# Kernel optimization log

Hardware: AMD Instinct MI355X
Metric: run time of the kernel (lower is better)

Reference implementation:

```python
import jax, jax.numpy as jnp
import numpy as np

D = 1024      # n_embd
NH = 16       # attention heads
E = 8         # n_experts
K = 2         # k_best
FF = 4 * D    # expert MLP hidden
EPS = 1e-6    # rms_norm_epsilon
TEMP = 1.0    # target_temperature


def setup_inputs() -> dict:
    key = jax.random.key(0)
    ks = jax.random.split(key, 12)
    B, S = 2, 1024
    s = 0.02
    return {
        "x": jax.random.normal(ks[0], (B, S, D), jnp.float32),
        "attn_norm_w": jnp.ones((D,), jnp.float32),
        "wq": jax.random.normal(ks[1], (D, D), jnp.float32) * s,
        "wk": jax.random.normal(ks[2], (D, D), jnp.float32) * s,
        "wv": jax.random.normal(ks[3], (D, D), jnp.float32) * s,
        "wo": jax.random.normal(ks[4], (D, D), jnp.float32) * s,
        "mlp_norm_w": jnp.ones((D,), jnp.float32),
        "router_w": jax.random.normal(ks[5], (D, E), jnp.float32) * s,
        "w1": jax.random.normal(ks[6], (E, D, FF), jnp.float32) * s,
        "b1": jnp.zeros((E, FF), jnp.float32),
        "w2": jax.random.normal(ks[7], (E, FF, D), jnp.float32) * s,
        "b2": jnp.zeros((E, D), jnp.float32),
    }


def _rmsnorm(x, w):
    var = jnp.mean(jnp.square(x), axis=-1, keepdims=True)
    return x * jax.lax.rsqrt(var + EPS) * w


def _attention(x, wq, wk, wv, wo):
    B, S, _ = x.shape
    dh = D // NH
    q = (x @ wq).reshape(B, S, NH, dh)
    k = (x @ wk).reshape(B, S, NH, dh)
    v = (x @ wv).reshape(B, S, NH, dh)
    scores = jnp.einsum("bqhd,bkhd->bhqk", q, k) / jnp.sqrt(jnp.float32(dh))
    causal = jnp.tril(jnp.ones((S, S), bool))  # [S,S]
    scores = jnp.where(causal[None, None], scores, jnp.finfo(scores.dtype).min)
    attn = jax.nn.softmax(scores, axis=-1)
    out = jnp.einsum("bhqk,bkhd->bqhd", attn, v).reshape(B, S, D)
    return out @ wo


def reference(x, attn_norm_w, wq, wk, wv, wo, mlp_norm_w, router_w, w1, b1, w2, b2):
    B, S, _ = x.shape
    # attention sub-block
    x = x + _attention(_rmsnorm(x, attn_norm_w), wq, wk, wv, wo)
    residual = x
    h = _rmsnorm(x, mlp_norm_w)  # [B,S,D]

    # router: temperature softmax + top-k
    logits = h @ router_w / TEMP                      # [B,S,E]
    probs = jax.nn.softmax(logits, axis=-1)
    top_k_scores, top_k_indices = jax.lax.top_k(probs, K)  # [B,S,K]
    onehot = jax.nn.one_hot(top_k_indices, E, dtype=h.dtype)  # [B,S,K,E]
    gates = jnp.einsum("bsk,bske->bse", top_k_scores, onehot)  # [B,S,E]

    # load-balancing loss (Switch-style) + expert counts
    counts = jnp.sum(onehot, axis=(0, 1, 2))          # [E]
    frac = counts / (B * S * K)
    mean_prob = jnp.mean(probs, axis=(0, 1))          # [E]
    balancing_loss = E * jnp.sum(frac * mean_prob)

    # experts: dense dispatch; tokens with zero gate contribute nothing,
    # so this matches the sort/gather/scatter top-k combine exactly.
    pre = jnp.einsum("bsd,edf->ebsf", h, w1) + b1[:, None, None]  # [E,B,S,FF]
    act = jax.nn.gelu(pre)
    y = jnp.einsum("ebsf,efd->ebsd", act, w2) + b2[:, None, None]  # [E,B,S,D]
    moe = jnp.einsum("ebsd,bse->bsd", y, gates)

    out = residual + moe
    return out, balancing_loss, counts
```

## Files before the change

kernel.cpp:

```cpp
#include <hip/hip_runtime.h>

typedef __bf16 bf16;
typedef __bf16 bf16x8 __attribute__((ext_vector_type(8)));
typedef float f32x4 __attribute__((ext_vector_type(4)));

#define D_   1024
#define S_   1024
#define B_   2
#define NTOK 2048
#define FF_  4096
#define NE   8
#define CAP  5120
#define OUTN 2097152

__device__ __forceinline__ float gelu_f(float x) {
    float u = 0.7978845608028654f * (x + 0.044715f * x * x * x);
    float a = fabsf(u);
    float e = __expf(-2.0f * a);
    float t = (1.0f - e) / (1.0f + e);
    t = copysignf(t, u);
    return 0.5f * x * (1.0f + t);
}

__device__ __forceinline__ void gload16(const void* g, void* l) {
    __builtin_amdgcn_global_load_lds((const __attribute__((address_space(1))) unsigned int*)g,
                                     (__attribute__((address_space(3))) unsigned int*)l,
                                     16, 0, 0);
}

__global__ __launch_bounds__(256) void rmsnorm_k(const float* __restrict__ x,
                                                 const float* __restrict__ w,
                                                 float* __restrict__ yf,
                                                 bf16* __restrict__ yhi,
                                                 bf16* __restrict__ ylo) {
    int row = blockIdx.x;
    int t = threadIdx.x;
    const float* xr = x + (size_t)row * D_;
    float4 v = *(const float4*)(xr + t * 4);
    float ss = v.x * v.x + v.y * v.y + v.z * v.z + v.w * v.w;
    for (int off = 32; off; off >>= 1) ss += __shfl_down(ss, off);
    __shared__ float wsum[4];
    if ((t & 63) == 0) wsum[t >> 6] = ss;
    __syncthreads();
    float tot = wsum[0] + wsum[1] + wsum[2] + wsum[3];
    float rr = rsqrtf(tot * (1.0f / D_) + 1e-6f);
    float4 wv = *(const float4*)(w + t * 4);
    float y[4];
    y[0] = v.x * rr * wv.x; y[1] = v.y * rr * wv.y;
    y[2] = v.z * rr * wv.z; y[3] = v.w * rr * wv.w;
    if (yf) *(float4*)(yf + (size_t)row * D_ + t * 4) = *(float4*)y;
    if (yhi) {
#pragma unroll
        for (int i = 0; i < 4; i++) {
            bf16 hi = (bf16)y[i];
            yhi[(size_t)row * D_ + t * 4 + i] = hi;
            if (ylo) ylo[(size_t)row * D_ + t * 4 + i] = (bf16)(y[i] - (float)hi);
        }
    }
}

__global__ __launch_bounds__(256) void trans_split_k(
    const float* __restrict__ w0, const float* __restrict__ w1p,
    const float* __restrict__ w2p, const float* __restrict__ w3,
    bf16* o0h, bf16* o0l, bf16* o1h, bf16* o1l,
    bf16* o2h, bf16* o2l, bf16* o3h, bf16* o3l) {
    int z = blockIdx.z;
    const float* src = (z == 0) ? w0 : (z == 1) ? w1p : (z == 2) ? w2p : w3;
    bf16* dh = (z == 0) ? o0h : (z == 1) ? o1h : (z == 2) ? o2h : o3h;
    bf16* dl = (z == 0) ? o0l : (z == 1) ? o1l : (z == 2) ? o2l : o3l;
    __shared__ float tl[32][33];
    int c0 = blockIdx.x * 32, r0 = blockIdx.y * 32;
    int tx = threadIdx.x & 31, ty = threadIdx.x >> 5;
#pragma unroll
    for (int i = 0; i < 4; i++) {
        int r = ty + i * 8;
        tl[r][tx] = src[(size_t)(r0 + r) * 1024 + c0 + tx];
    }
    __syncthreads();
#pragma unroll
    for (int i = 0; i < 4; i++) {
        int c = ty + i * 8;
        float v = tl[tx][c];
        bf16 hi = (bf16)v;
        dh[(size_t)(c0 + c) * 1024 + r0 + tx] = hi;
        dl[(size_t)(c0 + c) * 1024 + r0 + tx] = (bf16)(v - (float)hi);
    }
}

__global__ __launch_bounds__(256) void transpose_cast_k(const float* __restrict__ in,
                                                        bf16* __restrict__ out,
                                                        int R, int C) {
    __shared__ float tl[32][33];
    size_t base = (size_t)blockIdx.z * R * C;
    const float* src = in + base;
    bf16* dst = out + base;
    int c0 = blockIdx.x * 32, r0 = blockIdx.y * 32;
    int tx = threadIdx.x & 31, tyy = threadIdx.x >> 5;
#pragma unroll
    for (int i = 0; i < 4; i++) {
        int r = tyy + i * 8;
        tl[r][tx] = src[(size_t)(r0 + r) * C + c0 + tx];
    }
    __syncthreads();
#pragma unroll
    for (int i = 0; i < 4; i++) {
        int c = tyy + i * 8;
        dst[(size_t)(c0 + c) * R + r0 + tx] = (bf16)tl[tx][c];
    }
}

#define SPLIT_STAGE(bi, k0)                             \
    gload16(gah0 + (k0), Lah[bi] + wv * 512);           \
    gload16(gah1 + (k0), Lah[bi] + 2048 + wv * 512);    \
    gload16(gal0 + (k0), Lal[bi] + wv * 512);           \
    gload16(gal1 + (k0), Lal[bi] + 2048 + wv * 512);    \
    gload16(gbh0 + (k0), Lbh[bi] + wv * 512);           \
    gload16(gbh1 + (k0), Lbh[bi] + 2048 + wv * 512);    \
    gload16(gbl0 + (k0), Lbl[bi] + wv * 512);           \
    gload16(gbl1 + (k0), Lbl[bi] + 2048 + wv * 512);

#define SPLIT_COMPUTE(bi) {                                                            \
    bf16x8 fah[4], fal[4], fbh[4], fbl[4];                                             \
    _Pragma("unroll") for (int i = 0; i < 4; i++) {                                    \
        fah[i] = *(const bf16x8*)(Lah[bi] + ra_off[i]);                                \
        fal[i] = *(const bf16x8*)(Lal[bi] + ra_off[i]);                                \
        fbh[i] = *(const bf16x8*)(Lbh[bi] + rb_off[i]);                                \
        fbl[i] = *(const bf16x8*)(Lbl[bi] + rb_off[i]);                                \
    }                                                                                  \
    _Pragma("unroll") for (int mt = 0; mt < 4; mt++)                                   \
    _Pragma("unroll") for (int nt = 0; nt < 4; nt++) {                                 \
        acc[mt][nt] = __builtin_amdgcn_mfma_f32_16x16x32_bf16(fah[mt], fbh[nt], acc[mt][nt], 0, 0, 0); \
        acc[mt][nt] = __builtin_amdgcn_mfma_f32_16x16x32_bf16(fah[mt], fbl[nt], acc[mt][nt], 0, 0, 0); \
        acc[mt][nt] = __builtin_amdgcn_mfma_f32_16x16x32_bf16(fal[mt], fbh[nt], acc[mt][nt], 0, 0, 0); \
    } }

#define GEMM128_SPLIT_BODY(EPILOGUE)                                                   \
    __shared__ __align__(16) bf16 Lah[2][4096];                                        \
    __shared__ __align__(16) bf16 Lal[2][4096];                                        \
    __shared__ __align__(16) bf16 Lbh[2][4096];                                        \
    __shared__ __align__(16) bf16 Lbl[2][4096];                                        \
    int t = threadIdx.x;                                                               \
    int wv = t >> 6, ln = t & 63;                                                      \
    int wm = wv >> 1, wn = wv & 1, l15 = ln & 15, qd = ln >> 4;                        \
    int sr0 = t >> 2, sr1 = 64 + sr0, cl = t & 3;                                      \
    int cs0 = (cl ^ ((sr0 >> 1) & 3)) * 8;                                             \
    int cs1 = (cl ^ ((sr1 >> 1) & 3)) * 8;                                             \
    const bf16* gah0 = Ah + (size_t)(m0 + sr0) * 1024 + cs0;                           \
    const bf16* gah1 = Ah + (size_t)(m0 + sr1) * 1024 + cs1;                           \
    const bf16* gal0 = Al + (size_t)(m0 + sr0) * 1024 + cs0;                           \
    const bf16* gal1 = Al + (size_t)(m0 + sr1) * 1024 + cs1;                           \
    const bf16* gbh0 = Bh + (size_t)(n0 + sr0) * 1024 + cs0;                           \
    const bf16* gbh1 = Bh + (size_t)(n0 + sr1) * 1024 + cs1;                           \
    const bf16* gbl0 = Bl + (size_t)(n0 + sr0) * 1024 + cs0;                           \
    const bf16* gbl1 = Bl + (size_t)(n0 + sr1) * 1024 + cs1;                           \
    int ra_off[4], rb_off[4];                                                          \
    _Pragma("unroll") for (int i = 0; i < 4; i++) {                                    \
        int r1 = wm * 64 + i * 16 + l15;                                               \
        ra_off[i] = r1 * 32 + (qd ^ ((r1 >> 1) & 3)) * 8;                              \
        int r2 = wn * 64 + i * 16 + l15;                                               \
        rb_off[i] = r2 * 32 + (qd ^ ((r2 >> 1) & 3)) * 8;                              \
    }                                                                                  \
    f32x4 acc[4][4];                                                                   \
    _Pragma("unroll") for (int mt = 0; mt < 4; mt++)                                   \
    _Pragma("unroll") for (int nt = 0; nt < 4; nt++) acc[mt][nt] = (f32x4){0.f,0.f,0.f,0.f}; \
    SPLIT_STAGE(0, 0);                                                                 \
    __syncthreads();                                                                   \
    for (int k0 = 0; k0 < 1024; k0 += 64) {                                            \
        SPLIT_STAGE(1, k0 + 32);                                                       \
        SPLIT_COMPUTE(0);                                                              \
        __syncthreads();                                                               \
        if (k0 + 64 < 1024) { SPLIT_STAGE(0, k0 + 64); }                               \
        SPLIT_COMPUTE(1);                                                              \
        __syncthreads();                                                               \
    }                                                                                  \
    _Pragma("unroll") for (int mt = 0; mt < 4; mt++)                                   \
    _Pragma("unroll") for (int nt = 0; nt < 4; nt++)                                   \
        _Pragma("unroll") for (int r = 0; r < 4; r++) {                                \
            int gm = m0 + wm * 64 + mt * 16 + qd * 4 + r;                              \
            int gn = n0 + wn * 64 + nt * 16 + l15;                                     \
            float vv = acc[mt][nt][r];                                                 \
            EPILOGUE                                                                   \
        }

__global__ __launch_bounds__(256) void gemm_qkv_k(
    const bf16* __restrict__ Ah, const bf16* __restrict__ Al,
    const bf16* __restrict__ Bqh, const bf16* __restrict__ Bql,
    const bf16* __restrict__ Bkh, const bf16* __restrict__ Bkl,
    const bf16* __restrict__ Bvh, const bf16* __restrict__ Bvl,
    bf16* Cqh, bf16* Cql, bf16* Ckh, bf16* Ckl, bf16* Cvh, bf16* Cvl) {
    int gy = blockIdx.y, zw = gy >> 3;
    const bf16* Bh = (zw == 0) ? Bqh : (zw == 1) ? Bkh : Bvh;
    const bf16* Bl = (zw == 0) ? Bql : (zw == 1) ? Bkl : Bvl;
    bf16* Ch = (zw == 0) ? Cqh : (zw == 1) ? Ckh : Cvh;
    bf16* Cl = (zw == 0) ? Cql : (zw == 1) ? Ckl : Cvl;
    int m0 = blockIdx.x * 128, n0 = (gy & 7) * 128;
    GEMM128_SPLIT_BODY({
        bf16 hi = (bf16)vv;
        Ch[(size_t)gm * D_ + gn] = hi;
        Cl[(size_t)gm * D_ + gn] = (bf16)(vv - (float)hi);
    })
}

__global__ __launch_bounds__(256) void gemm_wo_k(
    const bf16* __restrict__ Ah, const bf16* __restrict__ Al,
    const bf16* __restrict__ Bh, const bf16* __restrict__ Bl,
    float* __restrict__ C, const float* __restrict__ X) {
    int m0 = blockIdx.x * 128, n0 = blockIdx.y * 128;
    GEMM128_SPLIT_BODY({
        C[(size_t)gm * D_ + gn] = X[(size_t)gm * D_ + gn] + vv;
    })
}

#define AP 72

__global__ __launch_bounds__(256) void attn_mfma_k(
    const bf16* __restrict__ qhp, const bf16* __restrict__ qlp,
    const bf16* __restrict__ khp, const bf16* __restrict__ klp,
    const bf16* __restrict__ vhp, const bf16* __restrict__ vlp,
    bf16* __restrict__ aoh, bf16* __restrict__ aol) {
    int qt = (int)gridDim.x - 1 - (int)blockIdx.x;
    int h = blockIdx.y, b = blockIdx.z;
    __shared__ bf16 Ksh[64 * AP], Ksl[64 * AP], VTh[64 * AP], VTl[64 * AP];
    __shared__ bf16 Ph[4][16 * AP], Pl[4][16 * AP];
    int t = threadIdx.x, wv = t >> 6, ln = t & 63, l15 = ln & 15, qd = ln >> 4;

    bf16x8 aqh[2], aql[2];
    {
        size_t qb = ((size_t)(b * S_ + qt * 64 + wv * 16 + l15)) * D_ + h * 64 + qd * 8;
        aqh[0] = *(const bf16x8*)(qhp + qb);
        aqh[1] = *(const bf16x8*)(qhp + qb + 32);
        aql[0] = *(const bf16x8*)(qlp + qb);
        aql[1] = *(const bf16x8*)(qlp + qb + 32);
    }
    f32x4 oacc[4];
    float mrow[4], lrow[4];
#pragma unroll
    for (int i = 0; i < 4; i++) {
        oacc[i] = (f32x4){0.f, 0.f, 0.f, 0.f};
        mrow[i] = -1e30f; lrow[i] = 0.0f;
    }

    for (int kt = 0; kt <= qt; kt++) {
        __syncthreads();
#pragma unroll
        for (int j = 0; j < 2; j++) {
            int idx = t + j * 256;
            int row = idx >> 3, ch = (idx & 7) * 8;
            size_t g = ((size_t)(b * S_ + kt * 64 + row)) * D_ + h * 64 + ch;
            *(bf16x8*)&Ksh[row * AP + ch] = *(const bf16x8*)(khp + g);
            *(bf16x8*)&Ksl[row * AP + ch] = *(const bf16x8*)(klp + g);
            bf16x8 vvh = *(const bf16x8*)(vhp + g);
            bf16x8 vvl = *(const bf16x8*)(vlp + g);
#pragma unroll
            for (int jj = 0; jj < 8; jj++) {
                VTh[(ch + jj) * AP + row] = vvh[jj];
                VTl[(ch + jj) * AP + row] = vvl[jj];
            }
        }
        __syncthreads();

        f32x4 sacc[4];
#pragma unroll
        for (int nt = 0; nt < 4; nt++) sacc[nt] = (f32x4){0.f, 0.f, 0.f, 0.f};
#pragma unroll
        for (int ks = 0; ks < 2; ks++) {
#pragma unroll
            for (int nt = 0; nt < 4; nt++) {
                bf16x8 bh = *(const bf16x8*)&Ksh[(nt * 16 + l15) * AP + ks * 32 + qd * 8];
                bf16x8 bl = *(const bf16x8*)&Ksl[(nt * 16 + l15) * AP + ks * 32 + qd * 8];
                sacc[nt] = __builtin_amdgcn_mfma_f32_16x16x32_bf16(aqh[ks], bh, sacc[nt], 0, 0, 0);
                sacc[nt] = __builtin_amdgcn_mfma_f32_16x16x32_bf16(aqh[ks], bl, sacc[nt], 0, 0, 0);
                sacc[nt] = __builtin_amdgcn_mfma_f32_16x16x32_bf16(aql[ks], bh, sacc[nt], 0, 0, 0);
            }
        }
        bool diag = (kt == qt);
#pragma unroll
        for (int r = 0; r < 4; r++) {
            float s0[4];
#pragma unroll
            for (int nt = 0; nt < 4; nt++) {
                s0[nt] = sacc[nt][r] * 0.125f;
                if (diag && (nt * 16 + l15) > (wv * 16 + qd * 4 + r)) s0[nt] = -1e30f;
            }
            float vmax = fmaxf(fmaxf(s0[0], s0[1]), fmaxf(s0[2], s0[3]));
            for (int off = 1; off < 16; off <<= 1) vmax = fmaxf(vmax, __shfl_xor(vmax, off));
            float mnew = fmaxf(mrow[r], vmax);
            float alpha = __expf(mrow[r] - mnew);
            float p[4], rs = 0.0f;
#pragma unroll
            for (int nt = 0; nt < 4; nt++) { p[nt] = __expf(s0[nt] - mnew); rs += p[nt]; }
            for (int off = 1; off < 16; off <<= 1) rs += __shfl_xor(rs, off);
            lrow[r] = lrow[r] * alpha + rs;
            mrow[r] = mnew;
#pragma unroll
            for (int nt = 0; nt < 4; nt++) oacc[nt][r] *= alpha;
            int prow = qd * 4 + r;
#pragma unroll
            for (int nt = 0; nt < 4; nt++) {
                bf16 hi = (bf16)p[nt];
                Ph[wv][prow * AP + nt * 16 + l15] = hi;
                Pl[wv][prow * AP + nt * 16 + l15] = (bf16)(p[nt] - (float)hi);
            }
        }
#pragma unroll
        for (int ks2 = 0; ks2 < 2; ks2++) {
            bf16x8 aph = *(const bf16x8*)&Ph[wv][l15 * AP + ks2 * 32 + qd * 8];
            bf16x8 apl = *(const bf16x8*)&Pl[wv][l15 * AP + ks2 * 32 + qd * 8];
#pragma unroll
            for (int nt = 0; nt < 4; nt++) {
                bf16x8 bvh = *(const bf16x8*)&VTh[(nt * 16 + l15) * AP + ks2 * 32 + qd * 8];
                bf16x8 bvl = *(const bf16x8*)&VTl[(nt * 16 + l15) * AP + ks2 * 32 + qd * 8];
                oacc[nt] = __builtin_amdgcn_mfma_f32_16x16x32_bf16(aph, bvh, oacc[nt], 0, 0, 0);
                oacc[nt] = __builtin_amdgcn_mfma_f32_16x16x32_bf16(aph, bvl, oacc[nt], 0, 0, 0);
                oacc[nt] = __builtin_amdgcn_mfma_f32_16x16x32_bf16(apl, bvh, oacc[nt], 0, 0, 0);
            }
        }
    }

#pragma unroll
    for (int r = 0; r < 4; r++) {
        float inv = 1.0f / lrow[r];
        size_t rowa = ((size_t)(b * S_ + qt * 64 + wv * 16 + qd * 4 + r)) * D_ + h * 64;
#pragma unroll
        for (int nt = 0; nt < 4; nt++) {
            float o = oacc[nt][r] * inv;
            bf16 hi = (bf16)o;
            aoh[rowa + nt * 16 + l15] = hi;
            aol[rowa + nt * 16 + l15] = (bf16)(o - (float)hi);
        }
    }
}

__global__ __launch_bounds__(256) void router_k(const float* __restrict__ h,
                                                const float* __restrict__ rw,
                                                int* __restrict__ tidx,
                                                float* __restrict__ tgate,
                                                int* __restrict__ ecnt,
                                                float* __restrict__ psum) {
    int wv = threadIdx.x >> 6, ln = threadIdx.x & 63;
    int tok = blockIdx.x * 4 + wv;
    const float* hr = h + (size_t)tok * D_;
    float acc[NE];
#pragma unroll
    for (int e = 0; e < NE; e++) acc[e] = 0.0f;
    int base = ln * 16;
#pragma unroll
    for (int c = 0; c < 4; c++) {
        float4 hv = *(const float4*)(hr + base + c * 4);
        const float* rp = rw + (size_t)(base + c * 4) * NE;
        float hx[4] = {hv.x, hv.y, hv.z, hv.w};
#pragma unroll
        for (int jj = 0; jj < 4; jj++)
#pragma unroll
            for (int e = 0; e < NE; e++)
                acc[e] = fmaf(hx[jj], rp[jj * NE + e], acc[e]);
    }
#pragma unroll
    for (int e = 0; e < NE; e++)
        for (int off = 32; off; off >>= 1) acc[e] += __shfl_down(acc[e], off);

    __shared__ float pb[4][NE];
    if (ln == 0) {
        float mx = acc[0];
#pragma unroll
        for (int e = 1; e < NE; e++) mx = fmaxf(mx, acc[e]);
        float p[NE], ssum = 0.0f;
#pragma unroll
        for (int e = 0; e < NE; e++) { p[e] = expf(acc[e] - mx); ssum += p[e]; }
        float inv = 1.0f / ssum;
#pragma unroll
        for (int e = 0; e < NE; e++) p[e] *= inv;
        int i0 = 0; float b0 = p[0];
#pragma unroll
        for (int e = 1; e < NE; e++) if (p[e] > b0) { b0 = p[e]; i0 = e; }
        int i1 = -1; float b1v = -1.0f;
#pragma unroll
        for (int e = 0; e < NE; e++) if (e != i0 && p[e] > b1v) { b1v = p[e]; i1 = e; }
        tidx[tok * 2] = i0; tidx[tok * 2 + 1] = i1;
        tgate[tok * 2] = b0; tgate[tok * 2 + 1] = b1v;
        atomicAdd(&ecnt[i0], 1);
        atomicAdd(&ecnt[i1], 1);
#pragma unroll
        for (int e = 0; e < NE; e++) pb[wv][e] = p[e];
    }
    __syncthreads();
    if (threadIdx.x < NE) {
        float s2 = pb[0][threadIdx.x] + pb[1][threadIdx.x] + pb[2][threadIdx.x] + pb[3][threadIdx.x];
        atomicAdd(&psum[threadIdx.x], s2);
    }
}

__global__ void passb_k(const int* __restrict__ ecnt, const float* __restrict__ psum,
                        int* __restrict__ eoffp, int* __restrict__ ecnt2,
                        float* __restrict__ out_tail) {
    if (threadIdx.x == 0) {
        int off = 0; float loss = 0.0f;
        for (int e = 0; e < NE; e++) {
            eoffp[e] = off;
            int c = ecnt[e];
            off += (c + 127) & ~127;
            loss += (c * (1.0f / 4096.0f)) * (psum[e] * (1.0f / 2048.0f));
            out_tail[1 + e] = (float)c;
            ecnt2[e] = 0;
        }
        eoffp[NE] = off;
        out_tail[0] = 8.0f * loss;
    }
}

__global__ __launch_bounds__(256) void scatter_k(const int* __restrict__ tidx,
                                                 const int* __restrict__ eoffp,
                                                 int* __restrict__ ecnt2,
                                                 int* __restrict__ stok,
                                                 int* __restrict__ sidx) {
    int tok = blockIdx.x * 256 + threadIdx.x;
    for (int k = 0; k < 2; k++) {
        int e = tidx[tok * 2 + k];
        int pos = eoffp[e] + atomicAdd(&ecnt2[e], 1);
        stok[pos] = tok;
        sidx[tok * 2 + k] = pos;
    }
}

#define MOE_STAGE(bufA, bufB, k0)                       \
    gload16(ga0 + (k0), bufA + wv * 512);               \
    gload16(ga1 + (k0), bufA + 2048 + wv * 512);        \
    gload16(gb0 + (k0), bufB + wv * 512);               \
    gload16(gb1 + (k0), bufB + 2048 + wv * 512);

#define MOE_COMPUTE(bufA, bufB) {                                                      \
    bf16x8 af[4], bfr[4];                                                              \
    _Pragma("unroll") for (int i = 0; i < 4; i++) {                                    \
        af[i]  = *(const bf16x8*)(bufA + ra_off[i]);                                   \
        bfr[i] = *(const bf16x8*)(bufB + rb_off[i]);                                   \
    }                                                                                  \
    _Pragma("unroll") for (int mt = 0; mt < 4; mt++)                                   \
    _Pragma("unroll") for (int nt = 0; nt < 4; nt++)                                   \
        acc[mt][nt] = __builtin_amdgcn_mfma_f32_16x16x32_bf16(af[mt], bfr[nt], acc[mt][nt], 0, 0, 0); }

__global__ __launch_bounds__(256) void moe_gemm1_k(const bf16* __restrict__ hB,
                                                   const bf16* __restrict__ w1t,
                                                   const float* __restrict__ b1,
                                                   const int* __restrict__ eoffp,
                                                   const int* __restrict__ stok,
                                                   bf16* __restrict__ act) {
    int m0 = blockIdx.x * 128, n0 = blockIdx.y * 128;
    if (m0 >= eoffp[NE]) return;
    int e = 0;
#pragma unroll
    for (int i = 1; i < NE; i++) if (m0 >= eoffp[i]) e = i;

    __shared__ __align__(16) bf16 As[4096];
    __shared__ __align__(16) bf16 Bs[4096];
    int t = threadIdx.x;
    int wv = t >> 6, ln = t & 63;
    int wm = wv >> 1, wn = wv & 1, l15 = ln & 15, qd = ln >> 4;

    int sr0 = t >> 2, sr1 = 64 + sr0, cl = t & 3;
    int cs0 = (cl ^ ((sr0 >> 1) & 3)) * 8;
    int cs1 = (cl ^ ((sr1 >> 1) & 3)) * 8;
    const bf16* ga0 = hB + (size_t)stok[m0 + sr0] * D_ + cs0;
    const bf16* ga1 = hB + (size_t)stok[m0 + sr1] * D_ + cs1;
    const bf16* Bb = w1t + ((size_t)e * FF_ + n0) * D_;
    const bf16* gb0 = Bb + (size_t)sr0 * D_ + cs0;
    const bf16* gb1 = Bb + (size_t)sr1 * D_ + cs1;

    int ra_off[4], rb_off[4];
#pragma unroll
    for (int i = 0; i < 4; i++) {
        int r1 = wm * 64 + i * 16 + l15;
        ra_off[i] = r1 * 32 + (qd ^ ((r1 >> 1) & 3)) * 8;
        int r2 = wn * 64 + i * 16 + l15;
        rb_off[i] = r2 * 32 + (qd ^ ((r2 >> 1) & 3)) * 8;
    }

    f32x4 acc[4][4];
#pragma unroll
    for (int mt = 0; mt < 4; mt++)
#pragma unroll
        for (int nt = 0; nt < 4; nt++) acc[mt][nt] = (f32x4){0.f, 0.f, 0.f, 0.f};

    for (int k0 = 0; k0 < D_; k0 += 32) {
        __syncthreads();
        MOE_STAGE(As, Bs, k0);
        __syncthreads();
        MOE_COMPUTE(As, Bs);
    }

    const float* b1e = b1 + (size_t)e * FF_;
#pragma unroll
    for (int mt = 0; mt < 4; mt++)
#pragma unroll
        for (int nt = 0; nt < 4; nt++) {
            int gn = n0 + wn * 64 + nt * 16 + l15;
            float bias = b1e[gn];
#pragma unroll
            for (int r = 0; r < 4; r++) {
                int gm = m0 + wm * 64 + mt * 16 + qd * 4 + r;
                act[(size_t)gm * FF_ + gn] = (bf16)gelu_f(acc[mt][nt][r] + bias);
            }
        }
}

__global__ __launch_bounds__(256) void moe_gemm2_k(const bf16* __restrict__ act,
                                                   const bf16* __restrict__ w2t,
                                                   const float* __restrict__ b2,
                                                   const int* __restrict__ eoffp,
                                                   float* __restrict__ y) {
    int m0 = blockIdx.x * 128, n0 = blockIdx.y * 128;
    if (m0 >= eoffp[NE]) return;
    int e = 0;
#pragma unroll
    for (int i = 1; i < NE; i++) if (m0 >= eoffp[i]) e = i;

    __shared__ __align__(16) bf16 As[2][4096];
    __shared__ __align__(16) bf16 Bs[2][4096];
    int t = threadIdx.x;
    int wv = t >> 6, ln = t & 63;
    int wm = wv >> 1, wn = wv & 1, l15 = ln & 15, qd = ln >> 4;

    int sr0 = t >> 2, sr1 = 64 + sr0, cl = t & 3;
    int cs0 = (cl ^ ((sr0 >> 1) & 3)) * 8;
    int cs1 = (cl ^ ((sr1 >> 1) & 3)) * 8;
    const bf16* ga0 = act + (size_t)(m0 + sr0) * FF_ + cs0;
    const bf16* ga1 = act + (size_t)(m0 + sr1) * FF_ + cs1;
    const bf16* Bb = w2t + ((size_t)e * D_ + n0) * FF_;
    const bf16* gb0 = Bb + (size_t)sr0 * FF_ + cs0;
    const bf16* gb1 = Bb + (size_t)sr1 * FF_ + cs1;

    int ra_off[4], rb_off[4];
#pragma unroll
    for (int i = 0; i < 4; i++) {
        int r1 = wm * 64 + i * 16 + l15;
        ra_off[i] = r1 * 32 + (qd ^ ((r1 >> 1) & 3)) * 8;
        int r2 = wn * 64 + i * 16 + l15;
        rb_off[i] = r2 * 32 + (qd ^ ((r2 >> 1) & 3)) * 8;
    }

    f32x4 acc[4][4];
#pragma unroll
    for (int mt = 0; mt < 4; mt++)
#pragma unroll
        for (int nt = 0; nt < 4; nt++) acc[mt][nt] = (f32x4){0.f, 0.f, 0.f, 0.f};

    MOE_STAGE(As[0], Bs[0], 0);
    __syncthreads();
    for (int k0 = 0; k0 < FF_; k0 += 64) {
        MOE_STAGE(As[1], Bs[1], k0 + 32);
        MOE_COMPUTE(As[0], Bs[0]);
        __syncthreads();
        if (k0 + 64 < FF_) { MOE_STAGE(As[0], Bs[0], k0 + 64); }
        MOE_COMPUTE(As[1], Bs[1]);
        __syncthreads();
    }

    const float* b2e = b2 + (size_t)e * D_;
#pragma unroll
    for (int mt = 0; mt < 4; mt++)
#pragma unroll
        for (int nt = 0; nt < 4; nt++) {
            int gn = n0 + wn * 64 + nt * 16 + l15;
            float bias = b2e[gn];
#pragma unroll
            for (int r = 0; r < 4; r++) {
                int gm = m0 + wm * 64 + mt * 16 + qd * 4 + r;
                y[(size_t)gm * D_ + gn] = acc[mt][nt][r] + bias;
            }
        }
}

__global__ __launch_bounds__(256) void combine_k(const float* __restrict__ y,
                                                 const int* __restrict__ sidx,
                                                 const float* __restrict__ tgate,
                                                 float* __restrict__ out) {
    int tok = blockIdx.x;
    int d = threadIdx.x * 4;
    int s0 = sidx[tok * 2], s1 = sidx[tok * 2 + 1];
    float g0 = tgate[tok * 2], g1 = tgate[tok * 2 + 1];
    float4 a = *(const float4*)(y + (size_t)s0 * D_ + d);
    float4 b = *(const float4*)(y + (size_t)s1 * D_ + d);
    float4 o = *(const float4*)(out + (size_t)tok * D_ + d);
    o.x += g0 * a.x + g1 * b.x;
    o.y += g0 * a.y + g1 * b.y;
    o.z += g0 * a.z + g1 * b.z;
    o.w += g0 * a.w + g1 * b.w;
    *(float4*)(out + (size_t)tok * D_ + d) = o;
}

extern "C" void kernel_launch(void* const* d_in, const int* in_sizes, int n_in,
                              void* d_out, int out_size, void* d_ws, size_t ws_size,
                              hipStream_t stream) {
    const float* x   = (const float*)d_in[0];
    const float* anw = (const float*)d_in[1];
    const float* wq  = (const float*)d_in[2];
    const float* wk  = (const float*)d_in[3];
    const float* wv  = (const float*)d_in[4];
    const float* wo  = (const float*)d_in[5];
    const float* mnw = (const float*)d_in[6];
    const float* rw  = (const float*)d_in[7];
    const float* w1  = (const float*)d_in[8];
    const float* b1  = (const float*)d_in[9];
    const float* w2  = (const float*)d_in[10];
    const float* b2  = (const float*)d_in[11];
    float* out = (float*)d_out;

    char* p = (char*)d_ws;
    auto take = [&](size_t n) { char* r = p; p += (n + 255) & ~(size_t)255; return r; };
    bf16* h1h = (bf16*)take((size_t)OUTN * 2);
    bf16* h1l = (bf16*)take((size_t)OUTN * 2);
    bf16* qh  = (bf16*)take((size_t)OUTN * 2);
    bf16* ql  = (bf16*)take((size_t)OUTN * 2);
    bf16* kh  = (bf16*)take((size_t)OUTN * 2);
    bf16* kl  = (bf16*)take((size_t)OUTN * 2);
    bf16* vh  = (bf16*)take((size_t)OUTN * 2);
    bf16* vl  = (bf16*)take((size_t)OUTN * 2);
    bf16* wqth = (bf16*)take((size_t)D_ * D_ * 2);
    bf16* wqtl = (bf16*)take((size_t)D_ * D_ * 2);
    bf16* wkth = (bf16*)take((size_t)D_ * D_ * 2);
    bf16* wktl = (bf16*)take((size_t)D_ * D_ * 2);
    bf16* wvth = (bf16*)take((size_t)D_ * D_ * 2);
    bf16* wvtl = (bf16*)take((size_t)D_ * D_ * 2);
    bf16* woth = (bf16*)take((size_t)D_ * D_ * 2);
    bf16* wotl = (bf16*)take((size_t)D_ * D_ * 2);
    bf16* w1t = (bf16*)take((size_t)NE * FF_ * D_ * 2);
    bf16* w2t = (bf16*)take((size_t)NE * FF_ * D_ * 2);
    bf16* act = (bf16*)take((size_t)CAP * FF_ * 2);
    int*   tidx  = (int*)take(NTOK * 2 * 4);
    float* tgate = (float*)take(NTOK * 2 * 4);
    int*   sidx  = (int*)take(NTOK * 2 * 4);
    int*   ecnt  = (int*)take(64);
    int*   ecnt2 = (int*)take(64);
    float* psum  = (float*)take(64);
    int*   eoffp = (int*)take(64);
    int*   stok  = (int*)take(CAP * 4);

    bf16*  aoh = h1h;
    bf16*  aol = h1l;
    float* h_f = (float*)qh;
    bf16*  h_b = kh;
    float* y   = (float*)vh;

    hipMemsetAsync(ecnt, 0, NE * 4, stream);
    hipMemsetAsync(psum, 0, NE * 4, stream);
    hipMemsetAsync(stok, 0, CAP * 4, stream);

    trans_split_k<<<dim3(32, 32, 4), 256, 0, stream>>>(wq, wk, wv, wo,
        wqth, wqtl, wkth, wktl, wvth, wvtl, woth, wotl);
    transpose_cast_k<<<dim3(FF_ / 32, D_ / 32, NE), 256, 0, stream>>>(w1, w1t, D_, FF_);
    transpose_cast_k<<<dim3(D_ / 32, FF_ / 32, NE), 256, 0, stream>>>(w2, w2t, FF_, D_);

    rmsnorm_k<<<NTOK, 256, 0, stream>>>(x, anw, nullptr, h1h, h1l);
    gemm_qkv_k<<<dim3(16, 24), 256, 0, stream>>>(h1h, h1l,
        wqth, wqtl, wkth, wktl, wvth, wvtl, qh, ql, kh, kl, vh, vl);
    attn_mfma_k<<<dim3(16, 16, 2), 256, 0, stream>>>(qh, ql, kh, kl, vh, vl, aoh, aol);
    gemm_wo_k<<<dim3(16, 8), 256, 0, stream>>>(aoh, aol, woth, wotl, out, x);

    rmsnorm_k<<<NTOK, 256, 0, stream>>>(out, mnw, h_f, h_b, nullptr);
    router_k<<<NTOK / 4, 256, 0, stream>>>(h_f, rw, tidx, tgate, ecnt, psum);
    passb_k<<<1, 64, 0, stream>>>(ecnt, psum, eoffp, ecnt2, out + OUTN);
    scatter_k<<<NTOK / 256, 256, 0, stream>>>(tidx, eoffp, ecnt2, stok, sidx);
    moe_gemm1_k<<<dim3(CAP / 128, FF_ / 128), 256, 0, stream>>>(h_b, w1t, b1, eoffp, stok, act);
    moe_gemm2_k<<<dim3(CAP / 128, D_ / 128), 256, 0, stream>>>(act, w2t, b2, eoffp, y);
    combine_k<<<NTOK, 256, 0, stream>>>(y, sidx, tgate, out);
}
```

Baseline: 814.3 us.

## Multi-stage async LDS pipelining with explicit vmcnt waits in MoE GEMMs

Both MoE expert GEMMs are rewritten to prefetch K-tiles into multiple LDS buffers using global_load_lds. Each step waits on a specific vmcnt count plus a raw s_barrier instead of __syncthreads, which drains all outstanding loads. GEMM1 moves from single-buffered to double-buffered, and GEMM2 from double to quad buffering, so loads stay in flight while the MFMAs run. In exchange, LDS use per block grows, which may cut occupancy, and correctness now depends on the hand-counted vmcnt values and loop bounds.

After: 790.6 us. 1.03x faster.

```diff
diff --git a/kernel.cpp b/kernel.cpp
--- a/kernel.cpp
+++ b/kernel.cpp
@@ -27,6 +27,11 @@
                                      (__attribute__((address_space(3))) unsigned int*)l,
                                      16, 0, 0);
 }
+
+#define VMCNT(n) asm volatile("s_waitcnt vmcnt(" n ")" ::: "memory")
+#define BARRIER() do { asm volatile("" ::: "memory"); \
+                       __builtin_amdgcn_s_barrier();  \
+                       asm volatile("" ::: "memory"); } while (0)
 
 __global__ __launch_bounds__(256) void rmsnorm_k(const float* __restrict__ x,
                                                  const float* __restrict__ w,
@@ -423,20 +428,26 @@
 }
 
 #define MOE_STAGE(bufA, bufB, k0)                       \
-    gload16(ga0 + (k0), bufA + wv * 512);               \
-    gload16(ga1 + (k0), bufA + 2048 + wv * 512);        \
-    gload16(gb0 + (k0), bufB + wv * 512);               \
-    gload16(gb1 + (k0), bufB + 2048 + wv * 512);
-
-#define MOE_COMPUTE(bufA, bufB) {                                                      \
+    gload16(ga0 + (k0), (bufA) + wv * 512);             \
+    gload16(ga1 + (k0), (bufA) + 2048 + wv * 512);      \
+    gload16(gb0 + (k0), (bufB) + wv * 512);             \
+    gload16(gb1 + (k0), (bufB) + 2048 + wv * 512);
+
+#define MOE_TILE(bufA, bufB) {                                                         \
     bf16x8 af[4], bfr[4];                                                              \
     _Pragma("unroll") for (int i = 0; i < 4; i++) {                                    \
-        af[i]  = *(const bf16x8*)(bufA + ra_off[i]);                                   \
-        bfr[i] = *(const bf16x8*)(bufB + rb_off[i]);                                   \
+        af[i]  = *(const bf16x8*)((bufA) + ra_off[i]);                                 \
+        bfr[i] = *(const bf16x8*)((bufB) + rb_off[i]);                                 \
     }                                                                                  \
     _Pragma("unroll") for (int mt = 0; mt < 4; mt++)                                   \
     _Pragma("unroll") for (int nt = 0; nt < 4; nt++)                                   \
         acc[mt][nt] = __builtin_amdgcn_mfma_f32_16x16x32_bf16(af[mt], bfr[nt], acc[mt][nt], 0, 0, 0); }
+
+#define MOE_STEP(rdA, rdB, VM)      \
+    VMCNT(VM);                      \
+    BARRIER();                      \
+    MOE_TILE(rdA, rdB);             \
+    BARRIER();
 
 __global__ __launch_bounds__(256) void moe_gemm1_k(const bf16* __restrict__ hB,
                                                    const bf16* __restrict__ w1t,
@@ -450,8 +461,8 @@
 #pragma unroll
     for (int i = 1; i < NE; i++) if (m0 >= eoffp[i]) e = i;
 
-    __shared__ __align__(16) bf16 As[4096];
-    __shared__ __align__(16) bf16 Bs[4096];
+    __shared__ __align__(16) bf16 As[2][4096];
+    __shared__ __align__(16) bf16 Bs[2][4096];
     int t = threadIdx.x;
     int wv = t >> 6, ln = t & 63;
     int wm = wv >> 1, wn = wv & 1, l15 = ln & 15, qd = ln >> 4;
@@ -480,12 +491,16 @@
 #pragma unroll
         for (int nt = 0; nt < 4; nt++) acc[mt][nt] = (f32x4){0.f, 0.f, 0.f, 0.f};
 
-    for (int k0 = 0; k0 < D_; k0 += 32) {
-        __syncthreads();
-        MOE_STAGE(As, Bs, k0);
-        __syncthreads();
-        MOE_COMPUTE(As, Bs);
-    }
+    MOE_STAGE(As[0], Bs[0], 0);
+    for (int k0 = 0; k0 < 960; k0 += 64) {
+        MOE_STAGE(As[1], Bs[1], k0 + 32);
+        MOE_STEP(As[0], Bs[0], "4");
+        MOE_STAGE(As[0], Bs[0], k0 + 64);
+        MOE_STEP(As[1], Bs[1], "4");
+    }
+    MOE_STAGE(As[1], Bs[1], 992);
+    MOE_STEP(As[0], Bs[0], "4");
+    MOE_STEP(As[1], Bs[1], "0");
 
     const float* b1e = b1 + (size_t)e * FF_;
 #pragma unroll
@@ -513,8 +528,8 @@
 #pragma unroll
     for (int i = 1; i < NE; i++) if (m0 >= eoffp[i]) e = i;
 
-    __shared__ __align__(16) bf16 As[2][4096];
-    __shared__ __align__(16) bf16 Bs[2][4096];
+    __shared__ __align__(16) bf16 As[4][4096];
+    __shared__ __align__(16) bf16 Bs[4][4096];
     int t = threadIdx.x;
     int wv = t >> 6, ln = t & 63;
     int wm = wv >> 1, wn = wv & 1, l15 = ln & 15, qd = ln >> 4;
@@ -544,15 +559,17 @@
         for (int nt = 0; nt < 4; nt++) acc[mt][nt] = (f32x4){0.f, 0.f, 0.f, 0.f};
 
     MOE_STAGE(As[0], Bs[0], 0);
-    __syncthreads();
-    for (int k0 = 0; k0 < FF_; k0 += 64) {
-        MOE_STAGE(As[1], Bs[1], k0 + 32);
-        MOE_COMPUTE(As[0], Bs[0]);
-        __syncthreads();
-        if (k0 + 64 < FF_) { MOE_STAGE(As[0], Bs[0], k0 + 64); }
-        MOE_COMPUTE(As[1], Bs[1]);
-        __syncthreads();
-    }
+    MOE_STAGE(As[1], Bs[1], 32);
+    for (int k0 = 0; k0 < 3968; k0 += 128) {
+        MOE_STAGE(As[2], Bs[2], k0 + 64);  MOE_STEP(As[0], Bs[0], "8");
+        MOE_STAGE(As[3], Bs[3], k0 + 96);  MOE_STEP(As[1], Bs[1], "8");
+        MOE_STAGE(As[0], Bs[0], k0 + 128); MOE_STEP(As[2], Bs[2], "8");
+        MOE_STAGE(As[1], Bs[1], k0 + 160); MOE_STEP(As[3], Bs[3], "8");
+    }
+    MOE_STAGE(As[2], Bs[2], 4032); MOE_STEP(As[0], Bs[0], "8");
+    MOE_STAGE(As[3], Bs[3], 4064); MOE_STEP(As[1], Bs[1], "8");
+    MOE_STEP(As[2], Bs[2], "4");
+    MOE_STEP(As[3], Bs[3], "0");
 
     const float* b2e = b2 + (size_t)e * D_;
 #pragma unroll
```
